# Performance work log

Hardware: AMD Instinct MI355X
Metric: run time of the kernel (lower is better)

The kernel has to match this reference:

```python
import jax, jax.numpy as jnp
import numpy as np

FEATURES, NEURONS, THETA, TAU, H = 128, 512, 256, 1.0, 0.1
B, T = 64, 2048

def setup_inputs() -> dict:
    key = jax.random.key(0)
    ks = jax.random.split(key, 8)
    IN = FEATURES + NEURONS
    s = lambda n: 1.0 / np.sqrt(n)
    return {
        "I": jax.random.normal(ks[0], (B, T, FEATURES), dtype=jnp.float32),
        "W_ih": jax.random.uniform(ks[1], (THETA, IN), jnp.float32, -s(THETA), s(THETA)),
        "W_hh": jax.random.uniform(ks[2], (THETA, THETA), jnp.float32, -s(THETA), s(THETA)),
        "b_ih": jax.random.uniform(ks[3], (THETA,), jnp.float32, -s(THETA), s(THETA)),
        "b_hh": jax.random.uniform(ks[4], (THETA,), jnp.float32, -s(THETA), s(THETA)),
        "W_out": jax.random.uniform(ks[5], (NEURONS, THETA), jnp.float32, -s(THETA), s(THETA)),
        "b_out": jax.random.uniform(ks[6], (NEURONS,), jnp.float32, -s(THETA), s(THETA)),
        "A": jax.random.normal(ks[7], (NEURONS,), dtype=jnp.float32),
    }

def reference(I, W_ih, W_hh, b_ih, b_hh, W_out, b_out, A):
    batch = I.shape[0]
    x0 = jnp.zeros((batch, NEURONS), I.dtype)
    s0 = jnp.zeros((batch, THETA), I.dtype)

    def step(carry, I_t):
        x, s = carry
        cat = jnp.concatenate([x, I_t], axis=-1)            # [B, neurons+features]
        s_new = jnp.tanh(cat @ W_ih.T + b_ih + s @ W_hh.T + b_hh)  # single-step tanh RNN
        f = jax.nn.relu(s_new @ W_out.T + b_out)            # [B, neurons]
        # implicit-Euler ODE update
        x_next = (x + H * (f * A)) / (1.0 + H * (1.0 / TAU + f))
        return (x_next, s_new), x_next

    _, xs = jax.lax.scan(step, (x0, s0), jnp.swapaxes(I, 0, 1))  # [T, B, neurons]
    return jnp.swapaxes(xs, 0, 1)  # [B, T, neurons]
```

## Files before the change

kernel.cpp:

```cpp
#include <hip/hip_runtime.h>
#include <hip/hip_fp16.h>

#define TT 2048
typedef unsigned int uint32;
typedef unsigned long long uint64;
typedef unsigned short ushort;

typedef _Float16 half2v __attribute__((ext_vector_type(2)));

#if defined(__has_builtin)
#  if __has_builtin(__builtin_amdgcn_fdot2)
#    define HAVE_DOT2 1
#  endif
#endif
#ifndef HAVE_DOT2
#  define HAVE_DOT2 0
#endif

#define WREG_N (2 * 176 * 512)
#define EX_N   (2 * 64 * 2 * 256)
#define ZQ_N   (2 * EX_N + 256)

__device__ __forceinline__ float dot2(uint32 a, uint32 w, float c)
{
#if HAVE_DOT2
    return __builtin_amdgcn_fdot2(__builtin_bit_cast(half2v, a),
                                  __builtin_bit_cast(half2v, w), c, false);
#else
    half2v av = __builtin_bit_cast(half2v, a);
    half2v wv = __builtin_bit_cast(half2v, w);
    c = fmaf((float)av.x, (float)wv.x, c);
    return fmaf((float)av.y, (float)wv.y, c);
#endif
}

__device__ __forceinline__ uint32 pkh(float a, float b)
{
    __half ha = __float2half(a), hb = __float2half(b);
    ushort ua = *reinterpret_cast<ushort*>(&ha);
    ushort ub = *reinterpret_cast<ushort*>(&hb);
    return (uint32)ua | ((uint32)ub << 16);
}

__device__ __forceinline__ float getSlice(const float* __restrict__ W_ih,
                                          const float* __restrict__ W_hh,
                                          int g, int j, int k)
{
    if (k < 256) return W_ih[j * 640 + 256 * g + k];
    if (k < 384) return W_hh[j * 256 + 128 * g + (k - 256)];
    return W_ih[j * 640 + 512 + 64 * g + (k - 384)];
}

__global__ void prep_kernel(const float* __restrict__ W_ih,
                            const float* __restrict__ W_hh,
                            const float* __restrict__ W_out,
                            uint32* __restrict__ WREGH,
                            uint64* __restrict__ zbase)
{
    int idx = blockIdx.x * blockDim.x + threadIdx.x;
    if (idx < WREG_N) {
        int tid  = idx & 511;
        int q    = idx >> 9;
        int g    = q / 176;
        int slot = q % 176;
        float lo, hi;
        if (slot < 112) {
            int j = tid >> 1, h = tid & 1;
            int k0 = 2 * (112 * h + slot);
            lo = getSlice(W_ih, W_hh, g, j, k0);
            hi = getSlice(W_ih, W_hh, g, j, k0 + 1);
        } else {
            int s  = slot - 112;
            int ii = s >> 2, m = s & 3;
            int nloc = tid >> 1, hh = tid & 1;
            int n  = 256 * g + nloc;
            int k0 = 128 * hh + 8 * ii + 2 * m;
            lo = W_out[n * 256 + k0];
            hi = W_out[n * 256 + k0 + 1];
        }
        WREGH[idx] = pkh(lo, hi);
    } else if (idx < WREG_N + ZQ_N) {
        zbase[idx - WREG_N] = 0ULL;
    }
}

__device__ __forceinline__ void bar_lds()
{
    asm volatile("s_waitcnt lgkmcnt(0)" ::: "memory");
    __builtin_amdgcn_s_barrier();
    asm volatile("" ::: "memory");
}

__device__ __forceinline__ void st64_sc0(uint64* p, uint64 v)
{
    asm volatile("global_store_dwordx2 %0, %1, off sc0" :: "v"(p), "v"(v) : "memory");
}
__device__ __forceinline__ uint64 ld64_sc0(const uint64* p)
{
    uint64 r;
    asm volatile("global_load_dwordx2 %0, %1, off sc0\n\ts_waitcnt vmcnt(0)"
                 : "=v"(r) : "v"(p) : "memory");
    return r;
}
__device__ __forceinline__ void st32_sc0(uint32* p, uint32 v)
{
    asm volatile("global_store_dword %0, %1, off sc0" :: "v"(p), "v"(v) : "memory");
}
__device__ __forceinline__ uint32 ld32_sc0(const uint32* p)
{
    uint32 r;
    asm volatile("global_load_dword %0, %1, off sc0\n\ts_waitcnt vmcnt(0)"
                 : "=v"(r) : "v"(p) : "memory");
    return r;
}

__global__ __launch_bounds__(512, 2)
void scan_kernel(const float* __restrict__ I,
                 const float* __restrict__ b_ih, const float* __restrict__ b_hh,
                 const float* __restrict__ b_out, const float* __restrict__ A,
                 const uint32* __restrict__ WREGH,
                 uint64* exS, uint64* exF, uint32* PS,
                 float* __restrict__ out)
{
    __shared__ uint4 apk4[2][56];
    __shared__ uint4 s4pk[32];
    __shared__ float xf32[256];
    __shared__ uint32 shInfo[2];

    const int tid = threadIdx.x;

    if (tid == 0) {
        uint32 x;
        asm volatile("s_getreg_b32 %0, hwreg(HW_REG_XCC_ID)" : "=s"(x));
        x &= 7u;
        uint32 rank = __hip_atomic_fetch_add(PS + x, 1u,
                          __ATOMIC_RELAXED, __HIP_MEMORY_SCOPE_AGENT);
        __hip_atomic_fetch_add(PS + 8, 1u, __ATOMIC_RELAXED, __HIP_MEMORY_SCOPE_AGENT);
        while (__hip_atomic_load(PS + 8, __ATOMIC_RELAXED, __HIP_MEMORY_SCOPE_AGENT) < 128u)
            __builtin_amdgcn_s_sleep(1);
        uint32 cnt[8];
        #pragma unroll
        for (int i = 0; i < 8; ++i)
            cnt[i] = __hip_atomic_load(PS + i, __ATOMIC_RELAXED, __HIP_MEMORY_SCOPE_AGENT);
        uint32 totp = 0, cumB = 0, sB = 0;
        #pragma unroll
        for (int i = 0; i < 8; ++i) {
            if ((uint32)i < x) { cumB += cnt[i] >> 1; sB += cnt[i] & 1; }
            totp += cnt[i] >> 1;
        }
        uint32 e, g;
        if (rank < 2u * (cnt[x] >> 1)) { e = cumB + (rank >> 1); g = rank & 1u; }
        else                           { e = totp + (sB >> 1);   g = sB & 1u; }
        uint32* pb = PS + 16  + 2 * e;
        uint32* vt = PS + 160 + 2 * e;
        const uint32 TOK = 0x5EEDF00Du;
        st32_sc0(pb + g, TOK);
        uint32 seen = 0;
        for (int it = 0; it < 4096 && !seen; ++it)
            seen = (ld32_sc0(pb + (1u - g)) == TOK) ? 1u : 0u;
        __hip_atomic_store(vt + g, seen ? 2u : 1u,
                           __ATOMIC_RELAXED, __HIP_MEMORY_SCOPE_AGENT);
        uint32 v0, v1;
        do {
            v0 = __hip_atomic_load(vt + 0, __ATOMIC_RELAXED, __HIP_MEMORY_SCOPE_AGENT);
            v1 = __hip_atomic_load(vt + 1, __ATOMIC_RELAXED, __HIP_MEMORY_SCOPE_AGENT);
        } while (v0 == 0u || v1 == 0u);
        shInfo[0] = e | (g << 16);
        shInfo[1] = (v0 == 2u && v1 == 2u) ? 1u : 0u;
    }
    __syncthreads();
    const int  e        = shInfo[0] & 0xffff;
    const int  g        = shInfo[0] >> 16;
    const bool fastpair = (shInfo[1] != 0);
    bool fastok = fastpair;

    uint32 wA[112], wB[64];
    const uint32* wsrc = WREGH + (size_t)g * (176 * 512) + tid;
    #pragma unroll
    for (int i = 0; i < 112; ++i) { wA[i] = wsrc[(size_t)i * 512]; asm("" : "+v"(wA[i])); }
    #pragma unroll
    for (int i = 0; i < 64;  ++i) { wB[i] = wsrc[(size_t)(112 + i) * 512]; asm("" : "+v"(wB[i])); }

    const int h    = tid & 1;
    const int jA   = tid >> 1;
    const int hh   = tid & 1;
    const int nloc = tid >> 1;

    const float bs   = ((tid & 1) == 0) ? (b_ih[jA] + b_hh[jA]) : 0.f;
    const float bo_r = ((tid & 1) == 0) ? b_out[256 * g + nloc] : 0.f;
    const float Av_r = ((tid & 1) == 0) ? A[256 * g + nloc] : 0.f;

    const size_t iBase   = (size_t)e * TT * 128 + 64 * g;
    const size_t outBase = (size_t)e * TT * 512 + 256 * g;

    {
        uint32* a0p = (uint32*)&apk4[0][0];
        if (tid < 192) a0p[tid] = 0u;
        else if (tid < 224) {
            int m = tid - 192;
            a0p[tid] = pkh(I[iBase + 2 * m], I[iBase + 2 * m + 1]);
        }
        if (tid < 256) xf32[tid] = 0.f;
    }
    __syncthreads();

    for (int t = 0; t < TT; ++t) {
        const int par = t & 1;
        const uint4* rdp = apk4[par];
        uint32*      wrp = (uint32*)apk4[par ^ 1];

        float2 iv2 = make_float2(0.f, 0.f);
        if (tid < 32) {
            int tl = (t + 1 < TT) ? (t + 1) : t;
            iv2 = *(const float2*)(I + iBase + (size_t)tl * 128 + 2 * tid);
        }

        float a0 = 0.f, a1 = 0.f;
        #pragma unroll
        for (int i = 0; i < 28; ++i) {
            uint4 av = rdp[28 * h + i];
            a0 = dot2(av.x, wA[4 * i + 0], a0);
            a1 = dot2(av.y, wA[4 * i + 1], a1);
            a0 = dot2(av.z, wA[4 * i + 2], a0);
            a1 = dot2(av.w, wA[4 * i + 3], a1);
        }
        float acc = a0 + a1;
        acc += __shfl_xor(acc, 1);

        const uint32 tgt   = (uint32)(t + 1);
        const size_t exoff = (size_t)(par * 64 + e) * (2 * 256);

        float sn = 0.f;
        if ((tid & 1) == 0) {
            uint64 u = ((uint64)tgt << 32) | (uint64)__float_as_uint(acc);
            if (fastpair) st64_sc0(exF + exoff + g * 256 + jA, u);
            __hip_atomic_store(exS + exoff + g * 256 + jA, u,
                               __ATOMIC_RELAXED, __HIP_MEMORY_SCOPE_AGENT);

            const uint64* fp = exF + exoff + (1 - g) * 256 + jA;
            const uint64* sp = exS + exoff + (1 - g) * 256 + jA;
            uint64 up = 0; bool got = false;
            if (fastok) {
                for (int it = 0; it < 1024 && !got; ++it) {
                    up = ld64_sc0(fp);
                    got = ((uint32)(up >> 32) == tgt);
                }
                if (!got) fastok = false;
            }
            while (!got) {
                up = __hip_atomic_load(sp, __ATOMIC_RELAXED, __HIP_MEMORY_SCOPE_AGENT);
                got = ((uint32)(up >> 32) == tgt);
            }

            float pre = acc + bs + __uint_as_float((uint32)up);
            float ex2 = __expf(2.f * pre);
            sn = 1.f - 2.f / (ex2 + 1.f);
        }
        {
            float sno = __shfl_xor(sn, 2);
            if ((tid & 3) == 0) {
                int p = tid >> 2;
                uint32 sp2 = pkh(sn, sno);
                ((uint32*)s4pk)[p] = sp2;
                int d = p - 64 * g;
                if (d >= 0 && d < 64) wrp[128 + d] = sp2;
            }
        }
        bar_lds();

        float c0 = 0.f, c1 = 0.f;
        #pragma unroll
        for (int i = 0; i < 16; ++i) {
            uint4 sv = s4pk[16 * hh + i];
            c0 = dot2(sv.x, wB[4 * i + 0], c0);
            c1 = dot2(sv.y, wB[4 * i + 1], c1);
            c0 = dot2(sv.z, wB[4 * i + 2], c0);
            c1 = dot2(sv.w, wB[4 * i + 3], c1);
        }
        float f = c0 + c1;
        f += __shfl_xor(f, 1);

        float xn = 0.f;
        if ((tid & 1) == 0) {
            float ff = fmaxf(f + bo_r, 0.f);
            float xo = xf32[nloc];
            xn = (xo + 0.1f * ff * Av_r) / (1.1f + 0.1f * ff);
            xf32[nloc] = xn;
            out[outBase + (size_t)t * 512 + nloc] = xn;
        }
        {
            float xno = __shfl_xor(xn, 2);
            if ((tid & 3) == 0)
                wrp[tid >> 2] = pkh(xn, xno);
        }
        if (tid < 32) wrp[192 + tid] = pkh(iv2.x, iv2.y);
        bar_lds();
    }
}

extern "C" void kernel_launch(void* const* d_in, const int* in_sizes, int n_in,
                              void* d_out, int out_size, void* d_ws, size_t ws_size,
                              hipStream_t stream)
{
    const float* I     = (const float*)d_in[0];
    const float* W_ih  = (const float*)d_in[1];
    const float* W_hh  = (const float*)d_in[2];
    const float* b_ih  = (const float*)d_in[3];
    const float* b_hh  = (const float*)d_in[4];
    const float* W_out = (const float*)d_in[5];
    const float* b_out = (const float*)d_in[6];
    const float* A     = (const float*)d_in[7];

    uint32* WREGH = (uint32*)d_ws;
    uint64* zbase = (uint64*)((uint32*)d_ws + WREG_N);
    uint64* exS   = zbase;
    uint64* exF   = zbase + EX_N;
    uint32* PS    = (uint32*)(zbase + 2 * EX_N);

    const int total = WREG_N + ZQ_N;
    prep_kernel<<<(total + 1023) / 1024, 1024, 0, stream>>>(W_ih, W_hh, W_out,
                                                            WREGH, zbase);
    scan_kernel<<<128, 512, 0, stream>>>(I, b_ih, b_hh, b_out, A,
                                         WREGH, exS, exF, PS, (float*)d_out);
}
```

Measured before the change: 4.876 ms.

## Use atomic ops for cross-block exchange, add accumulators, pad shared s buffer

Replaces the sc0 plain global loads and stores used for the fast inter-block exchange and pairing handshake with atomic swap and atomic add-zero reads, and changes the spin limits. It also splits each dot-product chain into four independent accumulators to shorten dependency chains, and pads the shared s4pk buffer so the two halves sit at different LDS offsets, presumably to avoid bank conflicts. Atomic reads go through L2 and may add latency per poll compared with the cached loads, and the reordered accumulation changes floating-point rounding slightly.

```diff
diff --git a/kernel.cpp b/kernel.cpp
--- a/kernel.cpp
+++ b/kernel.cpp
@@ -91,26 +91,28 @@
     asm volatile("" ::: "memory");
 }
 
-__device__ __forceinline__ void st64_sc0(uint64* p, uint64 v)
-{
-    asm volatile("global_store_dwordx2 %0, %1, off sc0" :: "v"(p), "v"(v) : "memory");
-}
-__device__ __forceinline__ uint64 ld64_sc0(const uint64* p)
+__device__ __forceinline__ void atom_sw64(uint64* p, uint64 v)
+{
+    asm volatile("global_atomic_swap_x2 %0, %1, off" :: "v"(p), "v"(v) : "memory");
+}
+__device__ __forceinline__ uint64 atom_rd64(uint64* p)
 {
     uint64 r;
-    asm volatile("global_load_dwordx2 %0, %1, off sc0\n\ts_waitcnt vmcnt(0)"
-                 : "=v"(r) : "v"(p) : "memory");
+    uint64 z = 0;
+    asm volatile("global_atomic_add_x2 %0, %1, %2, off sc0\n\ts_waitcnt vmcnt(0)"
+                 : "=&v"(r) : "v"(p), "v"(z) : "memory");
     return r;
 }
-__device__ __forceinline__ void st32_sc0(uint32* p, uint32 v)
-{
-    asm volatile("global_store_dword %0, %1, off sc0" :: "v"(p), "v"(v) : "memory");
-}
-__device__ __forceinline__ uint32 ld32_sc0(const uint32* p)
+__device__ __forceinline__ void atom_sw32(uint32* p, uint32 v)
+{
+    asm volatile("global_atomic_swap %0, %1, off" :: "v"(p), "v"(v) : "memory");
+}
+__device__ __forceinline__ uint32 atom_rd32(uint32* p)
 {
     uint32 r;
-    asm volatile("global_load_dword %0, %1, off sc0\n\ts_waitcnt vmcnt(0)"
-                 : "=v"(r) : "v"(p) : "memory");
+    uint32 z = 0;
+    asm volatile("global_atomic_add %0, %1, %2, off sc0\n\ts_waitcnt vmcnt(0)"
+                 : "=&v"(r) : "v"(p), "v"(z) : "memory");
     return r;
 }
 
@@ -123,7 +125,7 @@
                  float* __restrict__ out)
 {
     __shared__ uint4 apk4[2][56];
-    __shared__ uint4 s4pk[32];
+    __shared__ uint4 s4pk[34];
     __shared__ float xf32[256];
     __shared__ uint32 shInfo[2];
 
@@ -154,10 +156,10 @@
         uint32* pb = PS + 16  + 2 * e;
         uint32* vt = PS + 160 + 2 * e;
         const uint32 TOK = 0x5EEDF00Du;
-        st32_sc0(pb + g, TOK);
+        atom_sw32(pb + g, TOK);
         uint32 seen = 0;
-        for (int it = 0; it < 4096 && !seen; ++it)
-            seen = (ld32_sc0(pb + (1u - g)) == TOK) ? 1u : 0u;
+        for (int it = 0; it < 512 && !seen; ++it)
+            seen = (atom_rd32(pb + (1u - g)) == TOK) ? 1u : 0u;
         __hip_atomic_store(vt + g, seen ? 2u : 1u,
                            __ATOMIC_RELAXED, __HIP_MEMORY_SCOPE_AGENT);
         uint32 v0, v1;
@@ -215,16 +217,16 @@
             iv2 = *(const float2*)(I + iBase + (size_t)tl * 128 + 2 * tid);
         }
 
-        float a0 = 0.f, a1 = 0.f;
+        float a0 = 0.f, a1 = 0.f, a2 = 0.f, a3 = 0.f;
         #pragma unroll
         for (int i = 0; i < 28; ++i) {
             uint4 av = rdp[28 * h + i];
             a0 = dot2(av.x, wA[4 * i + 0], a0);
             a1 = dot2(av.y, wA[4 * i + 1], a1);
-            a0 = dot2(av.z, wA[4 * i + 2], a0);
-            a1 = dot2(av.w, wA[4 * i + 3], a1);
-        }
-        float acc = a0 + a1;
+            a2 = dot2(av.z, wA[4 * i + 2], a2);
+            a3 = dot2(av.w, wA[4 * i + 3], a3);
+        }
+        float acc = (a0 + a1) + (a2 + a3);
         acc += __shfl_xor(acc, 1);
 
         const uint32 tgt   = (uint32)(t + 1);
@@ -233,16 +235,16 @@
         float sn = 0.f;
         if ((tid & 1) == 0) {
             uint64 u = ((uint64)tgt << 32) | (uint64)__float_as_uint(acc);
-            if (fastpair) st64_sc0(exF + exoff + g * 256 + jA, u);
+            if (fastpair) atom_sw64(exF + exoff + g * 256 + jA, u);
             __hip_atomic_store(exS + exoff + g * 256 + jA, u,
                                __ATOMIC_RELAXED, __HIP_MEMORY_SCOPE_AGENT);
 
-            const uint64* fp = exF + exoff + (1 - g) * 256 + jA;
-            const uint64* sp = exS + exoff + (1 - g) * 256 + jA;
+            uint64* fp = exF + exoff + (1 - g) * 256 + jA;
+            uint64* sp = exS + exoff + (1 - g) * 256 + jA;
             uint64 up = 0; bool got = false;
             if (fastok) {
-                for (int it = 0; it < 1024 && !got; ++it) {
-                    up = ld64_sc0(fp);
+                for (int it = 0; it < 4096 && !got; ++it) {
+                    up = atom_rd64(fp);
                     got = ((uint32)(up >> 32) == tgt);
                 }
                 if (!got) fastok = false;
@@ -261,23 +263,23 @@
             if ((tid & 3) == 0) {
                 int p = tid >> 2;
                 uint32 sp2 = pkh(sn, sno);
-                ((uint32*)s4pk)[p] = sp2;
+                ((uint32*)s4pk)[p < 64 ? p : p + 4] = sp2;
                 int d = p - 64 * g;
                 if (d >= 0 && d < 64) wrp[128 + d] = sp2;
             }
         }
         bar_lds();
 
-        float c0 = 0.f, c1 = 0.f;
+        float c0 = 0.f, c1 = 0.f, c2 = 0.f, c3 = 0.f;
         #pragma unroll
         for (int i = 0; i < 16; ++i) {
-            uint4 sv = s4pk[16 * hh + i];
+            uint4 sv = s4pk[17 * hh + i];
             c0 = dot2(sv.x, wB[4 * i + 0], c0);
             c1 = dot2(sv.y, wB[4 * i + 1], c1);
-            c0 = dot2(sv.z, wB[4 * i + 2], c0);
-            c1 = dot2(sv.w, wB[4 * i + 3], c1);
-        }
-        float f = c0 + c1;
+            c2 = dot2(sv.z, wB[4 * i + 2], c2);
+            c3 = dot2(sv.w, wB[4 * i + 3], c3);
+        }
+        float f = (c0 + c1) + (c2 + c3);
         f += __shfl_xor(f, 1);
 
         float xn = 0.f;
```

Result: faster. 4.578 ms (-6.1%).
